# Kernel optimization log

Measured on AMD Instinct MI355X. Metric: run time of the kernel, lower is better.

The kernel has to match this reference:

```python
import jax, jax.numpy as jnp
import numpy as np

D = 256
H = 8
HD = D // H
K = 10
CAP = 500000
B = 256


def setup_inputs() -> dict:
    key = jax.random.key(0)
    ks = jax.random.split(key, 5)
    return {
        "content": jax.random.normal(ks[0], (B, D), dtype=jnp.float32),
        "hologram": jax.random.normal(ks[1], (CAP, D), dtype=jnp.float32),
        "memory_strengths": jnp.ones((CAP,), dtype=jnp.float32),
        "in_proj_w": jax.random.normal(ks[2], (3 * D, D), dtype=jnp.float32) * (1.0 / np.sqrt(D)),
        "in_proj_b": jnp.zeros((3 * D,), dtype=jnp.float32),
        "out_proj_w": jax.random.normal(ks[3], (D, D), dtype=jnp.float32) * (1.0 / np.sqrt(D)),
        "out_proj_b": jnp.zeros((D,), dtype=jnp.float32),
    }


def reference(content, hologram, memory_strengths, in_proj_w, in_proj_b, out_proj_w, out_proj_b):
    # similarities [B, CAP], weighted by per-slot memory strength
    sims = jnp.matmul(content, hologram.T) * memory_strengths[None, :]
    # top-k memory slots per query
    top_vals, top_idx = jax.lax.top_k(sims, K)            # [B, K]
    mem = hologram[top_idx]                               # gather -> [B, K, D]

    # nn.MultiheadAttention (batch_first): packed in-proj split into q/k/v
    wq, wk, wv = in_proj_w[:D], in_proj_w[D:2 * D], in_proj_w[2 * D:]
    bq, bk, bv = in_proj_b[:D], in_proj_b[D:2 * D], in_proj_b[2 * D:]

    q = content @ wq.T + bq                               # [B, D]  (query len 1)
    k = mem @ wk.T + bk                                   # [B, K, D]
    v = mem @ wv.T + bv                                   # [B, K, D]

    qh = q.reshape(B, H, HD)                              # [B, H, HD]
    kh = k.reshape(B, K, H, HD).transpose(0, 2, 1, 3)     # [B, H, K, HD]
    vh = v.reshape(B, K, H, HD).transpose(0, 2, 1, 3)     # [B, H, K, HD]

    scores = jnp.einsum("bhd,bhkd->bhk", qh, kh) / np.sqrt(HD)
    attn = jax.nn.softmax(scores, axis=-1)                # [B, H, K]
    ctx = jnp.einsum("bhk,bhkd->bhd", attn, vh).reshape(B, D)
    recalled = ctx @ out_proj_w.T + out_proj_b            # [B, D]

    # torch MHA returns head-averaged attention weights; query len 1 squeezed
    attn_weights = attn.mean(axis=1)                      # [B, K]
    return recalled, attn_weights
```

## Files before the change

### kernel.cpp

```cpp
#include <hip/hip_runtime.h>
#include <hip/hip_bf16.h>
#include <math.h>

#define D      256
#define H      8
#define HD     32
#define TOPK   10
#define CAP    500000
#define BATCH  256

#define G1     256
#define T1     512
#define NT     32
#define ROUNDS 62
#define CHUNK  (NT*ROUNDS)
#define TOPB   16
#define MSEL   32

typedef float  f32x16 __attribute__((ext_vector_type(16)));
typedef __bf16 bf16x8 __attribute__((ext_vector_type(8)));

union FragCvt { uint4 u; bf16x8 v; };

__device__ __forceinline__ unsigned bfpair(float lo, float hi){
  unsigned a = __builtin_bit_cast(unsigned, lo);
  unsigned b = __builtin_bit_cast(unsigned, hi);
  a += 0x7FFFu + ((a >> 16) & 1u);
  b += 0x7FFFu + ((b >> 16) & 1u);
  return (a >> 16) | (b & 0xFFFF0000u);
}
__device__ __forceinline__ uint4 pack8(float4 p0, float4 p1){
  uint4 u;
  u.x = bfpair(p0.x, p0.y); u.y = bfpair(p0.z, p0.w);
  u.z = bfpair(p1.x, p1.y); u.w = bfpair(p1.z, p1.w);
  return u;
}

__device__ __forceinline__ void list_insert(float (&tv)[TOPB], int (&ti)[TOPB],
                                            float &minv, int &mins, float v, int gi){
  #pragma unroll
  for (int q = 0; q < TOPB; ++q){ if (q == mins){ tv[q] = v; ti[q] = gi; } }
  float mv = tv[0]; int ms = 0;
  #pragma unroll
  for (int q = 1; q < TOPB; ++q){
    float x = tv[q];
    if (x < mv){ mv = x; ms = q; }
  }
  minv = mv; mins = ms;
}

#define ROUND_BODY(R, I0,I1,I2,I3,IS, S0,S1,S2,S3,SS)                               \
  do {                                                                              \
    {                                              \
      int g  = n0 + ((R)+2)*NT + srow;                                              \
      int gc = (g < CAP) ? g : (CAP-1);                                             \
      int gb = gc*64 + scol*4;                                                      \
      I0 = hf4[gb+0]; I1 = hf4[gb+1]; I2 = hf4[gb+2]; I3 = hf4[gb+3];               \
      if (t < NT){                                                                  \
        int sidx = n0 + ((R)+2)*NT + t;                                             \
        IS = stren[(sidx < CAP) ? sidx : (CAP-1)];                                  \
      }                                                                             \
    }                                                                               \
    {         \
      f32x16 acc = {0.f,0.f,0.f,0.f,0.f,0.f,0.f,0.f,                                \
                    0.f,0.f,0.f,0.f,0.f,0.f,0.f,0.f};                               \
      const int bbase = ml*32;                                                      \
      const int kxor  = ml & 7;                                                     \
      _Pragma("unroll")                                                             \
      for (int ks = 0; ks < 16; ++ks){                                              \
        FragCvt fb; fb.u = Bb[bufR][bbase + ((ks*2 + half) ^ kxor)];                \
        acc = __builtin_amdgcn_mfma_f32_32x32x16_bf16(fb.v, afrag[ks], acc, 0,0,0); \
      }                                                                             \
      \
      const float4* s4 = (const float4*)strenb[bufR];                               \
      float4 sg0 = s4[0 + half], sg1 = s4[2 + half],                                \
             sg2 = s4[4 + half], sg3 = s4[6 + half];                                \
      float sv[16];                                                                 \
      sv[ 0]=acc[ 0]*sg0.x; sv[ 1]=acc[ 1]*sg0.y; sv[ 2]=acc[ 2]*sg0.z;             \
      sv[ 3]=acc[ 3]*sg0.w; sv[ 4]=acc[ 4]*sg1.x; sv[ 5]=acc[ 5]*sg1.y;             \
      sv[ 6]=acc[ 6]*sg1.z; sv[ 7]=acc[ 7]*sg1.w; sv[ 8]=acc[ 8]*sg2.x;             \
      sv[ 9]=acc[ 9]*sg2.y; sv[10]=acc[10]*sg2.z; sv[11]=acc[11]*sg2.w;             \
      sv[12]=acc[12]*sg3.x; sv[13]=acc[13]*sg3.y; sv[14]=acc[14]*sg3.z;             \
      sv[15]=acc[15]*sg3.w;                                                         \
                 \
      const int nbase = n0 + (R)*NT;                                                \
      const bool full = (nbase + NT) <= CAP;                                        \
      unsigned pend = 0u;                                                           \
      _Pragma("unroll")                                                             \
      for (int j = 0; j < 16; ++j){                                                 \
        int offj = (j & 3) + 8*(j >> 2) + 4*half;                                   \
        bool ok = (sv[j] > minv) && (full || (nbase + offj) < CAP);                 \
        pend |= ok ? (1u << j) : 0u;                                                \
      }                                                                             \
      while (__any(pend != 0u)){                                                    \
        if (pend){                                                                  \
          int j = __builtin_ctz(pend);                                              \
          pend &= pend - 1u;                                                        \
          float v = -INFINITY;                                                      \
          _Pragma("unroll")                                                         \
          for (int q = 0; q < 16; ++q) v = (q == j) ? sv[q] : v;                    \
          if (v > minv){                                                            \
            int gi = nbase + (j & 3) + 8*(j >> 2) + 4*half;                         \
            list_insert(tv, ti, minv, mins, v, gi);                                 \
          }                                                                         \
        }                                                                           \
      }                                                                             \
    }                                                                               \
    {                   \
      int kc0 = scol*2;                                                             \
      Bb[bufW][srow*32 + ((kc0  ) ^ (srow&7))] = pack8(S0, S1);                     \
      Bb[bufW][srow*32 + ((kc0+1) ^ (srow&7))] = pack8(S2, S3);                     \
      if (t < NT) strenb[bufW][t] = SS;                                             \
    }                                                                               \
    __syncthreads();                                                                \
    bufR = (bufR == 2) ? 0 : bufR + 1;                                              \
    bufW = (bufW == 2) ? 0 : bufW + 1;                                              \
  } while (0)

__global__ __launch_bounds__(T1) void k_score(
    const float* __restrict__ content, const float* __restrict__ holo,
    const float* __restrict__ stren, float* __restrict__ cand_val,
    int* __restrict__ cand_idx)
{
  __shared__ uint4 Bb[3][NT*32];
  __shared__ float strenb[3][NT];

  const int t    = threadIdx.x;
  const int lane = t & 63;
  const int w    = t >> 6;
  const int half = lane >> 5;
  const int ml   = lane & 31;

  bf16x8 afrag[16];
  {
    const float4* cf4 = (const float4*)content;
    int base = (w*32 + ml)*64 + half*2;
    #pragma unroll
    for (int ks = 0; ks < 16; ++ks){
      float4 p0 = cf4[base + ks*4 + 0];
      float4 p1 = cf4[base + ks*4 + 1];
      FragCvt fc; fc.u = pack8(p0, p1);
      afrag[ks] = fc.v;
    }
  }

  float tv[TOPB]; int ti[TOPB];
  #pragma unroll
  for (int q = 0; q < TOPB; ++q){ tv[q] = -INFINITY; ti[q] = 0; }
  float minv = -INFINITY; int mins = 0;

  const int n0 = blockIdx.x * CHUNK;

  const int srow = t >> 4;
  const int scol = t & 15;
  const float4* hf4 = (const float4*)holo;

  float4 a0, a1, a2, a3, b0, b1, b2, b3;
  float  sa = 0.f, sb = 0.f;
  {
    int g  = n0 + srow;
    int gc = (g < CAP) ? g : (CAP-1);
    int gb = gc*64 + scol*4;
    a0 = hf4[gb+0]; a1 = hf4[gb+1]; a2 = hf4[gb+2]; a3 = hf4[gb+3];
    g  = n0 + NT + srow;
    gc = (g < CAP) ? g : (CAP-1);
    gb = gc*64 + scol*4;
    b0 = hf4[gb+0]; b1 = hf4[gb+1]; b2 = hf4[gb+2]; b3 = hf4[gb+3];
    if (t < NT){
      int s0 = n0 + t;
      sa = stren[(s0 < CAP) ? s0 : (CAP-1)];
      int s1 = n0 + NT + t;
      sb = stren[(s1 < CAP) ? s1 : (CAP-1)];
    }
    int kc0 = scol*2;
    Bb[0][srow*32 + ((kc0  ) ^ (srow&7))] = pack8(a0, a1);
    Bb[0][srow*32 + ((kc0+1) ^ (srow&7))] = pack8(a2, a3);
    if (t < NT) strenb[0][t] = sa;
  }
  __syncthreads();

  int bufR = 0, bufW = 1;
  for (int r = 0; r < ROUNDS; r += 2){
    ROUND_BODY(r,   a0,a1,a2,a3,sa,  b0,b1,b2,b3,sb);
    ROUND_BODY(r+1, b0,b1,b2,b3,sb,  a0,a1,a2,a3,sa);
  }

  #pragma unroll
  for (int q = 0; q < TOPB; ++q){
    float ov = __shfl_xor(tv[q], 32);
    int   oi = __shfl_xor(ti[q], 32);
    if (half == 0 && ov > minv) list_insert(tv, ti, minv, mins, ov, oi);
  }
  if (half == 0){
    int m    = w*32 + ml;
    int base = m*(G1*TOPB) + blockIdx.x*TOPB;
    #pragma unroll
    for (int q = 0; q < TOPB; ++q){
      cand_val[base+q] = tv[q];
      cand_idx[base+q] = ti[q];
    }
  }
}

__global__ void k_merge(const float* __restrict__ content,
                        const float* __restrict__ holo,
                        const float* __restrict__ stren,
                        const float* __restrict__ cand_val,
                        const int* __restrict__ cand_idx,
                        int* __restrict__ top_idx)
{
  const int row  = blockIdx.x;
  const int t    = threadIdx.x;
  const int lane = t & 63;
  const int w    = t >> 6;

  float cv[16]; int ci[16];
  {
    int base = row*(G1*TOPB);
    #pragma unroll
    for (int i = 0; i < 16; ++i){
      int c = i*256 + t;
      cv[i] = cand_val[base + c];
      ci[i] = cand_idx[base + c];
    }
  }
  __shared__ float  lv[4];
  __shared__ int    li[4];
  __shared__ int    sel[MSEL];
  __shared__ double ex[MSEL];
  __shared__ float  cont[D];

  for (int s = 0; s < MSEL; ++s){
    float bv = -INFINITY; int bi = 0x7FFFFFFF;
    #pragma unroll
    for (int i = 0; i < 16; ++i){
      if (cv[i] > bv || (cv[i] == bv && ci[i] < bi)){ bv = cv[i]; bi = ci[i]; }
    }
    #pragma unroll
    for (int off = 1; off < 64; off <<= 1){
      float ov = __shfl_xor(bv, off);
      int   oi = __shfl_xor(bi, off);
      if (ov > bv || (ov == bv && oi < bi)){ bv = ov; bi = oi; }
    }
    if (lane == 0){ lv[w] = bv; li[w] = bi; }
    __syncthreads();
    float wv = lv[0]; int wi = li[0];
    #pragma unroll
    for (int q = 1; q < 4; ++q){
      float ov = lv[q]; int oi = li[q];
      if (ov > wv || (ov == wv && oi < wi)){ wv = ov; wi = oi; }
    }
    if (t == 0) sel[s] = wi;
    #pragma unroll
    for (int i = 0; i < 16; ++i){ if (ci[i] == wi) cv[i] = -INFINITY; }
    __syncthreads();
  }
  if (t < 64) ((float4*)cont)[t] = ((const float4*)content)[row*64 + t];
  __syncthreads();

  const float4* hf4 = (const float4*)holo;
  float4 c4 = ((const float4*)cont)[lane];
  for (int q = 0; q < 8; ++q){
    int s   = w*8 + q;
    int idx = sel[s];
    float4 h4 = hf4[idx*64 + lane];
    double a = (double)h4.x*c4.x + (double)h4.y*c4.y + (double)h4.z*c4.z + (double)h4.w*c4.w;
    #pragma unroll
    for (int off = 1; off < 64; off <<= 1) a += __shfl_xor(a, off);
    if (lane == 0) ex[s] = a * (double)stren[idx];
  }
  __syncthreads();
  if (t == 0){
    unsigned used = 0;
    for (int r = 0; r < TOPK; ++r){
      int best = -1;
      for (int c = 0; c < MSEL; ++c){
        if (used & (1u << c)) continue;
        if (best < 0 || ex[c] > ex[best] || (ex[c] == ex[best] && sel[c] < sel[best])) best = c;
      }
      used |= (1u << best);
      top_idx[row*16 + r] = sel[best];
    }
  }
}

__global__ __launch_bounds__(512) void k_attn(
    const float* __restrict__ content, const float* __restrict__ holo,
    const float* __restrict__ inw, const float* __restrict__ inb,
    const float* __restrict__ outw, const float* __restrict__ outb,
    const int* __restrict__ top_idx, float* __restrict__ out)
{
  const int b = blockIdx.x;
  const int t = threadIdx.x;
  __shared__ float cont[D];
  __shared__ float mem_s[TOPK*D];
  __shared__ float q_s[D];
  __shared__ float k_s[TOPK*D];
  __shared__ float v_s[TOPK*D];
  __shared__ float sc[H*TOPK];
  __shared__ float at[H*TOPK];
  __shared__ float ctx[D];

  if (t < 64) ((float4*)cont)[t] = ((const float4*)content)[b*64 + t];
  for (int i = t; i < TOPK*D; i += 512){
    int j = i >> 8; int d = i & 255;
    mem_s[i] = holo[(size_t)top_idx[b*16 + j]*D + d];
  }
  __syncthreads();

  const float4* wf4 = (const float4*)inw;
  if (t < 256){
    float a = 0.f;
    const float4* c4p = (const float4*)cont;
    #pragma unroll 8
    for (int dc = 0; dc < 64; ++dc){
      float4 wv = wf4[t*64 + dc];
      float4 cc = c4p[dc];
      a += wv.x*cc.x + wv.y*cc.y + wv.z*cc.z + wv.w*cc.w;
    }
    q_s[t] = a + inb[t];
  }
  {
    int i    = (t < 256) ? t : (t - 256);
    int wrow = (t < 256) ? (256 + i) : (512 + i);
    float a[10];
    #pragma unroll
    for (int j = 0; j < 10; ++j) a[j] = 0.f;
    const float4* m4 = (const float4*)mem_s;
    for (int dc = 0; dc < 64; ++dc){
      float4 wv = wf4[wrow*64 + dc];
      #pragma unroll
      for (int j = 0; j < 10; ++j){
        float4 mm = m4[j*64 + dc];
        a[j] += wv.x*mm.x + wv.y*mm.y + wv.z*mm.z + wv.w*mm.w;
      }
    }
    float bias = inb[wrow];
    if (t < 256){
      #pragma unroll
      for (int j = 0; j < 10; ++j) k_s[j*256 + i] = a[j] + bias;
    } else {
      #pragma unroll
      for (int j = 0; j < 10; ++j) v_s[j*256 + i] = a[j] + bias;
    }
  }
  __syncthreads();
  if (t < H*TOPK){
    int h = t / TOPK, j = t % TOPK;
    float a = 0.f;
    #pragma unroll
    for (int d = 0; d < HD; ++d) a += q_s[h*HD + d] * k_s[j*256 + h*HD + d];
    sc[t] = a * 0.17677669529663687f;
  }
  __syncthreads();
  if (t < H){
    float m = -INFINITY;
    #pragma unroll
    for (int j = 0; j < 10; ++j) m = fmaxf(m, sc[t*10 + j]);
    float e[10]; float su = 0.f;
    #pragma unroll
    for (int j = 0; j < 10; ++j){ e[j] = expf(sc[t*10 + j] - m); su += e[j]; }
    float inv = 1.f / su;
    #pragma unroll
    for (int j = 0; j < 10; ++j) at[t*10 + j] = e[j]*inv;
  }
  __syncthreads();
  if (t < TOPK){
    float a = 0.f;
    #pragma unroll
    for (int h = 0; h < H; ++h) a += at[h*10 + t];
    out[BATCH*D + b*TOPK + t] = a * 0.125f;
  }
  if (t < 256){
    int h = t >> 5;
    float a = 0.f;
    #pragma unroll
    for (int j = 0; j < 10; ++j) a += at[h*10 + j] * v_s[j*256 + t];
    ctx[t] = a;
  }
  __syncthreads();
  if (t < 256){
    const float4* of4 = (const float4*)outw;
    const float4* c4p = (const float4*)ctx;
    float a = 0.f;
    #pragma unroll 8
    for (int dc = 0; dc < 64; ++dc){
      float4 wv = of4[t*64 + dc];
      float4 cc = c4p[dc];
      a += wv.x*cc.x + wv.y*cc.y + wv.z*cc.z + wv.w*cc.w;
    }
    out[b*D + t] = a + outb[t];
  }
}

extern "C" void kernel_launch(void* const* d_in, const int* in_sizes, int n_in,
                              void* d_out, int out_size, void* d_ws, size_t ws_size,
                              hipStream_t stream) {
  const float* content = (const float*)d_in[0];
  const float* holo    = (const float*)d_in[1];
  const float* stren   = (const float*)d_in[2];
  const float* inw     = (const float*)d_in[3];
  const float* inb     = (const float*)d_in[4];
  const float* outw    = (const float*)d_in[5];
  const float* outb    = (const float*)d_in[6];
  float* out = (float*)d_out;

  float* cand_val = (float*)d_ws;
  int*   cand_idx = (int*)(cand_val + BATCH*G1*TOPB);
  int*   top_idx  = (int*)(cand_idx + BATCH*G1*TOPB);

  hipLaunchKernelGGL(k_score, dim3(G1), dim3(T1), 0, stream,
                     content, holo, stren, cand_val, cand_idx);
  hipLaunchKernelGGL(k_merge, dim3(BATCH), dim3(256), 0, stream,
                     content, holo, stren, cand_val, cand_idx, top_idx);
  hipLaunchKernelGGL(k_attn, dim3(BATCH), dim3(512), 0, stream,
                     content, holo, inw, inb, outw, outb, top_idx, out);
}
```

Measured before the change: 940.4 us.

## Defer top-k insertion by one round to overlap with MFMA, use double buffer

The top-k insertion for the previous round's scores now runs while the current round's MFMA chain is in flight, so the selection work can hide the MFMA latency. The warp-uniform __any pending-mask loop is replaced with a simple per-element conditional insert. Shared buffers drop from triple to double buffering with compile-time buffer parity, which removes the runtime bufR/bufW rotation. The cost is 16 extra live registers for the deferred scores plus an epilogue that drains the last round, and the per-element branches may diverge more within a wave.

Measured after the change: 1.014 ms. 7.8% more time.

```diff
diff --git a/kernel.cpp b/kernel.cpp
--- a/kernel.cpp
+++ b/kernel.cpp
@@ -49,7 +49,7 @@
   minv = mv; mins = ms;
 }
 
-#define ROUND_BODY(R, I0,I1,I2,I3,IS, S0,S1,S2,S3,SS)                               \
+#define ROUND_BODY(R, PAR, I0,I1,I2,I3,IS, S0,S1,S2,S3,SS)                          \
   do {                                                                              \
     {                                              \
       int g  = n0 + ((R)+2)*NT + srow;                                              \
@@ -61,60 +61,46 @@
         IS = stren[(sidx < CAP) ? sidx : (CAP-1)];                                  \
       }                                                                             \
     }                                                                               \
-    {         \
-      f32x16 acc = {0.f,0.f,0.f,0.f,0.f,0.f,0.f,0.f,                                \
-                    0.f,0.f,0.f,0.f,0.f,0.f,0.f,0.f};                               \
+    f32x16 acc = {0.f,0.f,0.f,0.f,0.f,0.f,0.f,0.f,                                  \
+                  0.f,0.f,0.f,0.f,0.f,0.f,0.f,0.f};                                 \
+    {          \
       const int bbase = ml*32;                                                      \
       const int kxor  = ml & 7;                                                     \
       _Pragma("unroll")                                                             \
       for (int ks = 0; ks < 16; ++ks){                                              \
-        FragCvt fb; fb.u = Bb[bufR][bbase + ((ks*2 + half) ^ kxor)];                \
+        FragCvt fb; fb.u = Bb[PAR][bbase + ((ks*2 + half) ^ kxor)];                 \
         acc = __builtin_amdgcn_mfma_f32_32x32x16_bf16(fb.v, afrag[ks], acc, 0,0,0); \
       }                                                                             \
-      \
-      const float4* s4 = (const float4*)strenb[bufR];                               \
+    }                                                                               \
+        \
+    if ((R) > 0){                                                                   \
+      const int nbasep = n0 + ((R)-1)*NT;                                           \
+      const bool fullp = (nbasep + NT) <= CAP;                                      \
+      _Pragma("unroll")                                                             \
+      for (int j = 0; j < 16; ++j){                                                 \
+        const int offj = (j & 3) + 8*(j >> 2) + 4*half;                             \
+        bool ok = (svp[j] > minv) && (fullp || (nbasep + offj) < CAP);              \
+        if (ok) list_insert(tv, ti, minv, mins, svp[j], nbasep + offj);             \
+      }                                                                             \
+    }                                                                               \
+    {        \
+      const float4* s4 = (const float4*)strenb[PAR];                                \
       float4 sg0 = s4[0 + half], sg1 = s4[2 + half],                                \
              sg2 = s4[4 + half], sg3 = s4[6 + half];                                \
-      float sv[16];                                                                 \
-      sv[ 0]=acc[ 0]*sg0.x; sv[ 1]=acc[ 1]*sg0.y; sv[ 2]=acc[ 2]*sg0.z;             \
-      sv[ 3]=acc[ 3]*sg0.w; sv[ 4]=acc[ 4]*sg1.x; sv[ 5]=acc[ 5]*sg1.y;             \
-      sv[ 6]=acc[ 6]*sg1.z; sv[ 7]=acc[ 7]*sg1.w; sv[ 8]=acc[ 8]*sg2.x;             \
-      sv[ 9]=acc[ 9]*sg2.y; sv[10]=acc[10]*sg2.z; sv[11]=acc[11]*sg2.w;             \
-      sv[12]=acc[12]*sg3.x; sv[13]=acc[13]*sg3.y; sv[14]=acc[14]*sg3.z;             \
-      sv[15]=acc[15]*sg3.w;                                                         \
-                 \
-      const int nbase = n0 + (R)*NT;                                                \
-      const bool full = (nbase + NT) <= CAP;                                        \
-      unsigned pend = 0u;                                                           \
-      _Pragma("unroll")                                                             \
-      for (int j = 0; j < 16; ++j){                                                 \
-        int offj = (j & 3) + 8*(j >> 2) + 4*half;                                   \
-        bool ok = (sv[j] > minv) && (full || (nbase + offj) < CAP);                 \
-        pend |= ok ? (1u << j) : 0u;                                                \
-      }                                                                             \
-      while (__any(pend != 0u)){                                                    \
-        if (pend){                                                                  \
-          int j = __builtin_ctz(pend);                                              \
-          pend &= pend - 1u;                                                        \
-          float v = -INFINITY;                                                      \
-          _Pragma("unroll")                                                         \
-          for (int q = 0; q < 16; ++q) v = (q == j) ? sv[q] : v;                    \
-          if (v > minv){                                                            \
-            int gi = nbase + (j & 3) + 8*(j >> 2) + 4*half;                         \
-            list_insert(tv, ti, minv, mins, v, gi);                                 \
-          }                                                                         \
-        }                                                                           \
-      }                                                                             \
+      svp[ 0]=acc[ 0]*sg0.x; svp[ 1]=acc[ 1]*sg0.y; svp[ 2]=acc[ 2]*sg0.z;          \
+      svp[ 3]=acc[ 3]*sg0.w; svp[ 4]=acc[ 4]*sg1.x; svp[ 5]=acc[ 5]*sg1.y;          \
+      svp[ 6]=acc[ 6]*sg1.z; svp[ 7]=acc[ 7]*sg1.w; svp[ 8]=acc[ 8]*sg2.x;          \
+      svp[ 9]=acc[ 9]*sg2.y; svp[10]=acc[10]*sg2.z; svp[11]=acc[11]*sg2.w;          \
+      svp[12]=acc[12]*sg3.x; svp[13]=acc[13]*sg3.y; svp[14]=acc[14]*sg3.z;          \
+      svp[15]=acc[15]*sg3.w;                                                        \
     }                                                                               \
-    {                   \
+    {                  \
       int kc0 = scol*2;                                                             \
-      Bb[bufW][srow*32 + ((kc0  ) ^ (srow&7))] = pack8(S0, S1);                     \
-      Bb[bufW][srow*32 + ((kc0+1) ^ (srow&7))] = pack8(S2, S3);                     \
-      if (t < NT) strenb[bufW][t] = SS;                                             \
+      Bb[(PAR)^1][srow*32 + ((kc0  ) ^ (srow&7))] = pack8(S0, S1);                  \
+      Bb[(PAR)^1][srow*32 + ((kc0+1) ^ (srow&7))] = pack8(S2, S3);                  \
+      if (t < NT) strenb[(PAR)^1][t] = SS;                                          \
     }                                                                               \
     __syncthreads();                                                                \
-    bufR = (bufR == 2) ? 0 : bufR + 1;                                              \
-    bufW = (bufW == 2) ? 0 : bufW + 1;                                              \
   } while (0)
 
 __global__ __launch_bounds__(T1) void k_score(
@@ -122,8 +108,8 @@
     const float* __restrict__ stren, float* __restrict__ cand_val,
     int* __restrict__ cand_idx)
 {
-  __shared__ uint4 Bb[3][NT*32];
-  __shared__ float strenb[3][NT];
+  __shared__ uint4 Bb[2][NT*32];
+  __shared__ float strenb[2][NT];
 
   const int t    = threadIdx.x;
   const int lane = t & 63;
@@ -148,6 +134,10 @@
   #pragma unroll
   for (int q = 0; q < TOPB; ++q){ tv[q] = -INFINITY; ti[q] = 0; }
   float minv = -INFINITY; int mins = 0;
+
+  float svp[16];
+  #pragma unroll
+  for (int j = 0; j < 16; ++j) svp[j] = -INFINITY;
 
   const int n0 = blockIdx.x * CHUNK;
 
@@ -179,10 +169,19 @@
   }
   __syncthreads();
 
-  int bufR = 0, bufW = 1;
   for (int r = 0; r < ROUNDS; r += 2){
-    ROUND_BODY(r,   a0,a1,a2,a3,sa,  b0,b1,b2,b3,sb);
-    ROUND_BODY(r+1, b0,b1,b2,b3,sb,  a0,a1,a2,a3,sa);
+    ROUND_BODY(r,   0, a0,a1,a2,a3,sa,  b0,b1,b2,b3,sb);
+    ROUND_BODY(r+1, 1, b0,b1,b2,b3,sb,  a0,a1,a2,a3,sa);
+  }
+  {
+    const int nbasep = n0 + (ROUNDS-1)*NT;
+    const bool fullp = (nbasep + NT) <= CAP;
+    #pragma unroll
+    for (int j = 0; j < 16; ++j){
+      const int offj = (j & 3) + 8*(j >> 2) + 4*half;
+      bool ok = (svp[j] > minv) && (fullp || (nbasep + offj) < CAP);
+      if (ok) list_insert(tv, ti, minv, mins, svp[j], nbasep + offj);
+    }
   }
 
   #pragma unroll
```
